# Performance work log

Hardware: AMD Instinct MI355X
Metric: run time of the kernel (lower is better)

Reference implementation:

```python
import jax, jax.numpy as jnp
import numpy as np

BN_EPS = 1e-3  # keras BatchNormalization default epsilon


def setup_inputs() -> dict:
    key = jax.random.key(0)
    ks = jax.random.split(key, 7)
    B, W, D, H, C = 2, 32, 32, 32, 256
    x = jax.random.normal(ks[0], (B, W, D, H, C), dtype=jnp.float32)
    # Stacked params for the 4 branches: [query, key, judge, value]
    conv_w = jax.random.normal(ks[1], (4, C, C), dtype=jnp.float32) / np.sqrt(C).astype(np.float32)
    conv_b = jax.random.normal(ks[2], (4, C), dtype=jnp.float32) * 0.01
    bn_scale = 1.0 + 0.1 * jax.random.normal(ks[3], (4, C), dtype=jnp.float32)
    bn_offset = 0.1 * jax.random.normal(ks[4], (4, C), dtype=jnp.float32)
    bn_mean = 0.1 * jax.random.normal(ks[5], (4, C), dtype=jnp.float32)
    bn_var = jax.random.uniform(ks[6], (4, C), dtype=jnp.float32, minval=0.5, maxval=1.5)
    gamma = jnp.asarray(1e-4, dtype=jnp.float32)  # scalar residual scale (init 0.0001 in source)
    return dict(x=x, conv_w=conv_w, conv_b=conv_b, bn_scale=bn_scale,
                bn_offset=bn_offset, bn_mean=bn_mean, bn_var=bn_var, gamma=gamma)


def _branch(x, w, b, s, o, m, v):
    # Conv3D 1x1x1 == per-voxel channel mixing, then inference-mode BN, then ReLU
    y = jnp.einsum('bwdhc,cf->bwdhf', x, w) + b
    y = s * (y - m) * jax.lax.rsqrt(v + BN_EPS) + o
    return jax.nn.relu(y)


def reference(x, conv_w, conv_b, bn_scale, bn_offset, bn_mean, bn_var, gamma):
    B, W, D, H, C = x.shape
    N = W * D * H
    # Raw reshape (B,W,D,H,C) -> (B,C,N), matching keras Reshape((C,-1)) on channels-last layout
    def br(i):
        return _branch(x, conv_w[i], conv_b[i], bn_scale[i], bn_offset[i],
                       bn_mean[i], bn_var[i]).reshape(B, C, N)
    Q, K, J, V = br(0), br(1), br(2), br(3)
    m1 = jnp.matmul(K, jnp.swapaxes(Q, 1, 2))   # (B, C, C)
    m2 = jnp.matmul(K, jnp.swapaxes(J, 1, 2))   # (B, C, C)
    affinity = jax.nn.sigmoid(jnp.matmul(m1, m2))  # (B, C, C), sigmoid not softmax
    weights = jnp.matmul(affinity, V)           # (B, C, N)
    weights = weights.reshape(B, W, D, H, C)    # raw reshape back, as in source
    return gamma * weights + x
```

## Files before the change

### kernel.cpp

```cpp
#include <hip/hip_runtime.h>
#include <math.h>

typedef __attribute__((ext_vector_type(4))) float  f32x4;
typedef __attribute__((ext_vector_type(8))) short  s16x8;
typedef __attribute__((ext_vector_type(4))) short  s16x4;

#define BN_EPS 1e-3f

static constexpr int    CC    = 256;
static constexpr int    NVOX  = 32768;
static constexpr int    BATCH = 2;
static constexpr int    MTOT  = BATCH * NVOX;
static constexpr size_t ELEM_BR = (size_t)MTOT * CC;
static constexpr size_t SZ_BR   = ELEM_BR * 2;
static constexpr size_t WS_Q   = 0;
static constexpr size_t WS_K   = WS_Q  + SZ_BR;
static constexpr size_t WS_J   = WS_K  + SZ_BR;
static constexpr size_t WS_V   = WS_J  + SZ_BR;
static constexpr size_t WS_M1  = WS_V  + SZ_BR;
static constexpr size_t WS_M2  = WS_M1 + (size_t)BATCH*CC*CC*4;
static constexpr size_t WS_AFF = WS_M2 + (size_t)BATCH*CC*CC*4;
static constexpr size_t WS_WT  = WS_AFF + (size_t)BATCH*CC*CC*2;
static constexpr size_t WS_AB  = WS_WT + (size_t)4*CC*CC*2;
static constexpr size_t WS_P   = WS_AB + 2048*4;
static constexpr size_t WS_NEED_PART = WS_P + (size_t)4*64*65536*2;

__device__ __forceinline__ short f2bf(float f) {
  union { float f; unsigned u; } v; v.f = f;
  unsigned u = v.u + 0x7FFFu + ((v.u >> 16) & 1u);
  return (short)(u >> 16);
}
__device__ __forceinline__ float bf2f(short s) {
  union { unsigned u; float f; } v; v.u = ((unsigned)(unsigned short)s) << 16;
  return v.f;
}

__global__ __launch_bounds__(256) void k0_prep(
    const float* __restrict__ conv_w, const float* __restrict__ conv_b,
    const float* __restrict__ bn_s, const float* __restrict__ bn_o,
    const float* __restrict__ bn_m, const float* __restrict__ bn_v,
    char* __restrict__ ws)
{
  int t = blockIdx.x * 256 + threadIdx.x;
  ((float*)(ws + WS_M1))[t] = 0.f;
  int f = t >> 16, rem = t & 65535;
  int cin = rem >> 8, cout = rem & 255;
  ((short*)(ws + WS_WT))[f*65536 + cout*256 + cin] = f2bf(conv_w[t]);
  if (t < 1024) {
    float alpha = bn_s[t] * rsqrtf(bn_v[t] + BN_EPS);
    float beta  = alpha * (conv_b[t] - bn_m[t]) + bn_o[t];
    float* ab = (float*)(ws + WS_AB);
    ab[t] = alpha; ab[1024 + t] = beta;
  }
}

__global__ __launch_bounds__(256, 2) void k1_branches(
    const float* __restrict__ x, char* __restrict__ ws)
{
  __shared__ short As[64 * 256];
  __shared__ short Bs[64 * 256];
  __shared__ short Rs[64][72];

  const int tid = threadIdx.x;
  const int m0  = blockIdx.x * 64;
  const int lane = tid & 63, wid = tid >> 6;
  const int wm = wid >> 1, wn = wid & 1;
  const int lr = lane & 15, lg = lane >> 4;

  const short* Wt = (const short*)(ws + WS_WT);
  const float* ab = (const float*)(ws + WS_AB);

  #pragma unroll
  for (int it = 0; it < 16; ++it) {
    int idx = tid + 256 * it;
    int r = idx >> 6, c4 = (idx & 63) << 2;
    const float4 v = *(const float4*)(x + (size_t)(m0 + r) * 256 + c4);
    s16x4 s; s[0]=f2bf(v.x); s[1]=f2bf(v.y); s[2]=f2bf(v.z); s[3]=f2bf(v.w);
    int u = c4 >> 3;
    int swz = ((u ^ ((r & 7) << 2)) << 3) | (c4 & 7);
    *(s16x4*)&As[r * 256 + swz] = s;
  }

  {
    const short* Wf = Wt;
    #pragma unroll
    for (int i = 0; i < 8; ++i) {
      int slot = i * 256 + tid;
      int cout = slot >> 5, u = slot & 31;
      int usrc = u ^ ((cout & 7) << 2);
      const short* src = Wf + cout * 256 + usrc * 8;
      short* dst = Bs + (size_t)(i * 256 + wid * 64) * 8;
      __builtin_amdgcn_global_load_lds(
          (const __attribute__((address_space(1))) void*)src,
          (__attribute__((address_space(3))) void*)dst, 16, 0, 0);
    }
  }

  __syncthreads();

  for (int nt = 0; nt < 16; ++nt) {
    const int f  = nt >> 2;
    const int c0 = (nt & 3) * 64;

    f32x4 acc[2][2];
    #pragma unroll
    for (int a = 0; a < 2; ++a)
      #pragma unroll
      for (int b = 0; b < 2; ++b) { f32x4 z = {0.f,0.f,0.f,0.f}; acc[a][b] = z; }

    #pragma unroll
    for (int k0 = 0; k0 < 8; ++k0) {
      const int ua = k0 * 4 + lg;
      s16x8 af[2], bf[2];
      #pragma unroll
      for (int mi = 0; mi < 2; ++mi) {
        int r = wm*32 + mi*16 + lr;
        int uu = ua ^ ((r & 7) << 2);
        af[mi] = *(const s16x8*)&As[r * 256 + uu * 8];
      }
      #pragma unroll
      for (int nj = 0; nj < 2; ++nj) {
        int c = wn*32 + nj*16 + lr;
        int uu = ua ^ ((c & 7) << 2);
        bf[nj] = *(const s16x8*)&Bs[c * 256 + uu * 8];
      }
      #pragma unroll
      for (int mi = 0; mi < 2; ++mi)
        #pragma unroll
        for (int nj = 0; nj < 2; ++nj)
          acc[mi][nj] = __builtin_amdgcn_mfma_f32_16x16x32_bf16(
              bf[nj], af[mi], acc[mi][nj], 0, 0, 0);
    }

    __syncthreads();

    if (nt < 15) {
      const int fn  = (nt + 1) >> 2;
      const int c0n = ((nt + 1) & 3) * 64;
      const short* Wf = Wt + fn * 65536 + c0n * 256;
      #pragma unroll
      for (int i = 0; i < 8; ++i) {
        int slot = i * 256 + tid;
        int cout = slot >> 5, u = slot & 31;
        int usrc = u ^ ((cout & 7) << 2);
        const short* src = Wf + cout * 256 + usrc * 8;
        short* dst = Bs + (size_t)(i * 256 + wid * 64) * 8;
        __builtin_amdgcn_global_load_lds(
            (const __attribute__((address_space(1))) void*)src,
            (__attribute__((address_space(3))) void*)dst, 16, 0, 0);
      }
    }

    #pragma unroll
    for (int nj = 0; nj < 2; ++nj) {
      int c4b = c0 + wn*32 + nj*16 + lg*4;
      const f32x4 al = *(const f32x4*)&ab[f*256 + c4b];
      const f32x4 be = *(const f32x4*)&ab[1024 + f*256 + c4b];
      #pragma unroll
      for (int mi = 0; mi < 2; ++mi) {
        s16x4 s;
        #pragma unroll
        for (int ii = 0; ii < 4; ++ii) {
          float yv = al[ii] * acc[mi][nj][ii] + be[ii];
          yv = yv > 0.f ? yv : 0.f;
          s[ii] = f2bf(yv);
        }
        *(s16x4*)&Rs[wm*32 + mi*16 + lr][wn*32 + nj*16 + lg*4] = s;
      }
    }

    __syncthreads();

    short* Yf = (short*)(ws + (size_t)f * SZ_BR);
    #pragma unroll
    for (int it = 0; it < 2; ++it) {
      int idx = tid + 256 * it;
      int r = idx >> 3, c8 = (idx & 7) << 3;
      *(s16x8*)&Yf[(size_t)(m0 + r) * 256 + c0 + c8] = *(const s16x8*)&Rs[r][c8];
    }
  }
}

template<int PART>
__global__ __launch_bounds__(512, 2) void k2_m1m2(char* __restrict__ ws)
{
  __shared__ short Ks[2][16384];
  __shared__ short Xs[2][16384];

  const int tid = threadIdx.x;
  const int chunk = blockIdx.x;
  const int mat = blockIdx.y;
  const int b   = blockIdx.z;
  const size_t boff = (size_t)b * NVOX * CC;
  const short* Km = (const short*)(ws + WS_K) + boff;
  const short* Xm = (const short*)(ws + (mat ? WS_J : WS_Q)) + boff;

  const int lane = tid & 63, wid = tid >> 6;
  const int wm = wid >> 1, wn = wid & 1;
  const int lr = lane & 15, lg = lane >> 4;

  f32x4 acc[4][8];
  #pragma unroll
  for (int a = 0; a < 4; ++a)
    #pragma unroll
    for (int c = 0; c < 8; ++c) { f32x4 z = {0.f,0.f,0.f,0.f}; acc[a][c] = z; }

  {
    const int n0 = chunk * 512;
    #pragma unroll
    for (int i = 0; i < 4; ++i) {
      int slot = i * 512 + tid;
      int r = slot >> 3, u = slot & 7;
      int usrc = u ^ (r & 7);
      const size_t so = (size_t)r * NVOX + n0 + usrc * 8;
      short* dK = Ks[0] + (size_t)(i * 512 + wid * 64) * 8;
      short* dX = Xs[0] + (size_t)(i * 512 + wid * 64) * 8;
      __builtin_amdgcn_global_load_lds(
          (const __attribute__((address_space(1))) void*)(Km + so),
          (__attribute__((address_space(3))) void*)dK, 16, 0, 0);
      __builtin_amdgcn_global_load_lds(
          (const __attribute__((address_space(1))) void*)(Xm + so),
          (__attribute__((address_space(3))) void*)dX, 16, 0, 0);
    }
  }
  __syncthreads();

  for (int t = 0; t < 8; ++t) {
    const int cur = t & 1;
    if (t < 7) {
      const int n0n = chunk * 512 + (t + 1) * 64;
      const int nxt = cur ^ 1;
      #pragma unroll
      for (int i = 0; i < 4; ++i) {
        int slot = i * 512 + tid;
        int r = slot >> 3, u = slot & 7;
        int usrc = u ^ (r & 7);
        const size_t so = (size_t)r * NVOX + n0n + usrc * 8;
        short* dK = Ks[nxt] + (size_t)(i * 512 + wid * 64) * 8;
        short* dX = Xs[nxt] + (size_t)(i * 512 + wid * 64) * 8;
        __builtin_amdgcn_global_load_lds(
            (const __attribute__((address_space(1))) void*)(Km + so),
            (__attribute__((address_space(3))) void*)dK, 16, 0, 0);
        __builtin_amdgcn_global_load_lds(
            (const __attribute__((address_space(1))) void*)(Xm + so),
            (__attribute__((address_space(3))) void*)dX, 16, 0, 0);
      }
    }
    #pragma unroll
    for (int ks = 0; ks < 2; ++ks) {
      const int ua = ks * 4 + lg;
      s16x8 a[4], xf[8];
      #pragma unroll
      for (int mi = 0; mi < 4; ++mi) {
        int r = wm*64 + mi*16 + lr;
        a[mi] = *(const s16x8*)&Ks[cur][r * 64 + (ua ^ (r & 7)) * 8];
      }
      #pragma unroll
      for (int nj = 0; nj < 8; ++nj) {
        int r = wn*128 + nj*16 + lr;
        xf[nj] = *(const s16x8*)&Xs[cur][r * 64 + (ua ^ (r & 7)) * 8];
      }
      #pragma unroll
      for (int mi = 0; mi < 4; ++mi)
        #pragma unroll
        for (int nj = 0; nj < 8; ++nj)
          acc[mi][nj] = __builtin_amdgcn_mfma_f32_16x16x32_bf16(
              a[mi], xf[nj], acc[mi][nj], 0, 0, 0);
    }
    __syncthreads();
  }

  if (PART) {
    short* P = (short*)(ws + WS_P) + ((size_t)((mat*2 + b)*64 + chunk)) * 65536;
    #pragma unroll
    for (int mi = 0; mi < 4; ++mi)
      #pragma unroll
      for (int nj = 0; nj < 8; ++nj) {
        int i = wm*64 + mi*16 + lg*4;
        int j = wn*128 + nj*16 + lr;
        #pragma unroll
        for (int ii = 0; ii < 4; ++ii)
          P[(size_t)(i + ii) * 256 + j] = f2bf(acc[mi][nj][ii]);
      }
  } else {
    float* M = (float*)(ws + (mat ? WS_M2 : WS_M1)) + (size_t)b * CC * CC;
    #pragma unroll
    for (int mi = 0; mi < 4; ++mi)
      #pragma unroll
      for (int nj = 0; nj < 8; ++nj) {
        int i = wm*64 + mi*16 + lg*4;
        int j = wn*128 + nj*16 + lr;
        #pragma unroll
        for (int ii = 0; ii < 4; ++ii)
          atomicAdd(&M[(size_t)(i + ii) * 256 + j], acc[mi][nj][ii]);
      }
  }
}

__global__ __launch_bounds__(256) void k25_reduce(char* __restrict__ ws)
{
  int idx = blockIdx.x * 256 + threadIdx.x;
  int mb = idx >> 16;
  int ij = idx & 65535;
  const short* P = (const short*)(ws + WS_P) + ((size_t)mb * 64) * 65536 + ij;
  float s = 0.f;
  #pragma unroll 8
  for (int c = 0; c < 64; ++c)
    s += bf2f(P[(size_t)c * 65536]);
  float* dst = (float*)(ws + ((mb >> 1) ? WS_M2 : WS_M1)) + (size_t)(mb & 1) * 65536 + ij;
  *dst = s;
}

__global__ __launch_bounds__(256) void k3_aff(char* __restrict__ ws)
{
  const int j = threadIdx.x;
  const int i = blockIdx.x & 255;
  const int b = blockIdx.x >> 8;
  const float* m1 = (const float*)(ws + WS_M1) + (size_t)b * CC * CC;
  const float* m2 = (const float*)(ws + WS_M2) + (size_t)b * CC * CC;
  float z = 0.f;
  #pragma unroll 8
  for (int k = 0; k < 256; ++k)
    z = fmaf(m1[i*256 + k], m2[k*256 + j], z);
  float a = 1.f / (1.f + expf(-z));
  ((short*)(ws + WS_AFF))[(size_t)b*CC*CC + i*256 + j] = f2bf(a);
}

__global__ __launch_bounds__(512, 4) void k4_out(
    const float* __restrict__ x, const float* __restrict__ gamma_p,
    char* __restrict__ ws, float* __restrict__ out)
{
  __shared__ short affS[256][72];
  __shared__ short Vs[128][72];

  const int tid = threadIdx.x;
  const int n0 = blockIdx.x * 128;
  const int b  = blockIdx.y;
  const float gamma = gamma_p[0];
  const short* aff = (const short*)(ws + WS_AFF) + (size_t)b * CC * CC;
  const short* Vm  = (const short*)(ws + WS_V) + (size_t)b * NVOX * CC;

  const int lane = tid & 63, wid = tid >> 6;
  const int wi = wid >> 1, wn = wid & 1;
  const int lr = lane & 15, lg = lane >> 4;

  f32x4 acc[4][4];
  #pragma unroll
  for (int a = 0; a < 4; ++a)
    #pragma unroll
    for (int c = 0; c < 4; ++c) { f32x4 z = {0.f,0.f,0.f,0.f}; acc[a][c] = z; }

  for (int c0 = 0; c0 < 256; c0 += 64) {
    __syncthreads();
    #pragma unroll
    for (int it = 0; it < 4; ++it) {
      int idx = tid + 512 * it;
      int r = idx >> 3, c8 = (idx & 7) << 3;
      *(s16x8*)&affS[r][c8] = *(const s16x8*)&aff[(size_t)r * 256 + c0 + c8];
    }
    #pragma unroll
    for (int it = 0; it < 2; ++it) {
      int idx = tid + 512 * it;
      int t15 = idx & 15;
      int cc = idx >> 4, n8 = t15 << 3;
      s16x8 v = *(const s16x8*)&Vm[(size_t)(c0 + cc) * NVOX + n0 + n8];
      #pragma unroll
      for (int uu = 0; uu < 8; ++uu) {
        int u = (uu + t15) & 7;
        Vs[n8 + u][cc] = v[u];
      }
    }
    __syncthreads();
    #pragma unroll
    for (int ks = 0; ks < 2; ++ks) {
      s16x8 af[4], bv[4];
      #pragma unroll
      for (int mi = 0; mi < 4; ++mi)
        af[mi] = *(const s16x8*)&affS[wi*64 + mi*16 + lr][ks*32 + lg*8];
      #pragma unroll
      for (int nj = 0; nj < 4; ++nj)
        bv[nj] = *(const s16x8*)&Vs[wn*64 + nj*16 + lr][ks*32 + lg*8];
      #pragma unroll
      for (int mi = 0; mi < 4; ++mi)
        #pragma unroll
        for (int nj = 0; nj < 4; ++nj)
          acc[mi][nj] = __builtin_amdgcn_mfma_f32_16x16x32_bf16(
              bv[nj], af[mi], acc[mi][nj], 0, 0, 0);
    }
  }
  #pragma unroll
  for (int mi = 0; mi < 4; ++mi)
    #pragma unroll
    for (int nj = 0; nj < 4; ++nj) {
      int i = wi*64 + mi*16 + lr;
      int n = n0 + wn*64 + nj*16 + lg*4;
      size_t flat = (size_t)b * NVOX * CC + (size_t)i * NVOX + n;
      const float4 xv = *(const float4*)(x + flat);
      float4 o;
      o.x = gamma * acc[mi][nj][0] + xv.x;
      o.y = gamma * acc[mi][nj][1] + xv.y;
      o.z = gamma * acc[mi][nj][2] + xv.z;
      o.w = gamma * acc[mi][nj][3] + xv.w;
      *(float4*)(out + flat) = o;
    }
}

extern "C" void kernel_launch(void* const* d_in, const int* in_sizes, int n_in,
                              void* d_out, int out_size, void* d_ws, size_t ws_size,
                              hipStream_t stream)
{
  const float* x      = (const float*)d_in[0];
  const float* conv_w = (const float*)d_in[1];
  const float* conv_b = (const float*)d_in[2];
  const float* bn_s   = (const float*)d_in[3];
  const float* bn_o   = (const float*)d_in[4];
  const float* bn_m   = (const float*)d_in[5];
  const float* bn_v   = (const float*)d_in[6];
  const float* gamma  = (const float*)d_in[7];
  char*  ws  = (char*)d_ws;
  float* out = (float*)d_out;

  const bool part = ws_size >= WS_NEED_PART;

  k0_prep    <<<1024, 256, 0, stream>>>(conv_w, conv_b, bn_s, bn_o, bn_m, bn_v, ws);
  k1_branches<<<1024, 256, 0, stream>>>(x, ws);
  if (part) {
    k2_m1m2<1><<<dim3(64, 2, 2), 512, 0, stream>>>(ws);
    k25_reduce<<<1024, 256, 0, stream>>>(ws);
  } else {
    k2_m1m2<0><<<dim3(64, 2, 2), 512, 0, stream>>>(ws);
  }
  k3_aff     <<<512, 256, 0, stream>>>(ws);
  k4_out     <<<dim3(256, 2), 512, 0, stream>>>(x, gamma, ws, out);
}
```

Baseline: 166.6 us.

## Restructure branch GEMM with double-buffered weights, register-resident A, shuffle-based stores

```diff
diff --git a/kernel.cpp b/kernel.cpp
--- a/kernel.cpp
+++ b/kernel.cpp
@@ -34,6 +34,15 @@
   union { unsigned u; float f; } v; v.u = ((unsigned)(unsigned short)s) << 16;
   return v.f;
 }
+__device__ __forceinline__ unsigned long long packBN(f32x4 a, f32x4 al, f32x4 be) {
+  union { s16x4 v; unsigned long long u; } c;
+  #pragma unroll
+  for (int ii = 0; ii < 4; ++ii) {
+    float yv = al[ii] * a[ii] + be[ii];
+    c.v[ii] = f2bf(yv > 0.f ? yv : 0.f);
+  }
+  return c.u;
+}
 
 __global__ __launch_bounds__(256) void k0_prep(
     const float* __restrict__ conv_w, const float* __restrict__ conv_b,
@@ -54,130 +63,123 @@
   }
 }
 
-__global__ __launch_bounds__(256, 2) void k1_branches(
+__global__ __launch_bounds__(512, 1) void k1_branches(
     const float* __restrict__ x, char* __restrict__ ws)
 {
-  __shared__ short As[64 * 256];
-  __shared__ short Bs[64 * 256];
-  __shared__ short Rs[64][72];
+  __shared__ short As[128 * 256];
+  __shared__ short Bs[2][64 * 256];
 
   const int tid = threadIdx.x;
-  const int m0  = blockIdx.x * 64;
+  const int m0  = blockIdx.x * 128;
   const int lane = tid & 63, wid = tid >> 6;
-  const int wm = wid >> 1, wn = wid & 1;
+  const int rowg = wid >> 1, coutg = wid & 1;
   const int lr = lane & 15, lg = lane >> 4;
 
   const short* Wt = (const short*)(ws + WS_WT);
   const float* ab = (const float*)(ws + WS_AB);
 
   #pragma unroll
+  for (int i = 0; i < 4; ++i) {
+    int slot = i * 512 + tid;
+    int cout = slot >> 5, u = slot & 31;
+    int usrc = u ^ (cout & 7);
+    __builtin_amdgcn_global_load_lds(
+        (const __attribute__((address_space(1))) void*)(Wt + cout * 256 + usrc * 8),
+        (__attribute__((address_space(3))) void*)(&Bs[0][(i * 512 + wid * 64) * 8]),
+        16, 0, 0);
+  }
+
+  #pragma unroll
   for (int it = 0; it < 16; ++it) {
-    int idx = tid + 256 * it;
+    int idx = tid + 512 * it;
     int r = idx >> 6, c4 = (idx & 63) << 2;
     const float4 v = *(const float4*)(x + (size_t)(m0 + r) * 256 + c4);
     s16x4 s; s[0]=f2bf(v.x); s[1]=f2bf(v.y); s[2]=f2bf(v.z); s[3]=f2bf(v.w);
     int u = c4 >> 3;
-    int swz = ((u ^ ((r & 7) << 2)) << 3) | (c4 & 7);
+    int swz = ((u ^ (r & 7)) << 3) | (c4 & 7);
     *(s16x4*)&As[r * 256 + swz] = s;
   }
 
-  {
-    const short* Wf = Wt;
-    #pragma unroll
-    for (int i = 0; i < 8; ++i) {
-      int slot = i * 256 + tid;
-      int cout = slot >> 5, u = slot & 31;
-      int usrc = u ^ ((cout & 7) << 2);
-      const short* src = Wf + cout * 256 + usrc * 8;
-      short* dst = Bs + (size_t)(i * 256 + wid * 64) * 8;
-      __builtin_amdgcn_global_load_lds(
-          (const __attribute__((address_space(1))) void*)src,
-          (__attribute__((address_space(3))) void*)dst, 16, 0, 0);
-    }
-  }
-
   __syncthreads();
+
+  const int rA0 = rowg * 32 + lr, rA1 = rA0 + 16;
+#define LDA(R, K) (*(const s16x8*)&As[(R) * 256 + ((((K)*4 + lg) ^ ((R) & 7)) * 8)])
+  const s16x8 fa00 = LDA(rA0,0), fa01 = LDA(rA0,1), fa02 = LDA(rA0,2), fa03 = LDA(rA0,3);
+  const s16x8 fa04 = LDA(rA0,4), fa05 = LDA(rA0,5), fa06 = LDA(rA0,6), fa07 = LDA(rA0,7);
+  const s16x8 fa10 = LDA(rA1,0), fa11 = LDA(rA1,1), fa12 = LDA(rA1,2), fa13 = LDA(rA1,3);
+  const s16x8 fa14 = LDA(rA1,4), fa15 = LDA(rA1,5), fa16 = LDA(rA1,6), fa17 = LDA(rA1,7);
+#undef LDA
+
+  const int cB0 = coutg * 32 + lr, cB1 = cB0 + 16;
 
   for (int nt = 0; nt < 16; ++nt) {
     const int f  = nt >> 2;
     const int c0 = (nt & 3) * 64;
 
-    f32x4 acc[2][2];
-    #pragma unroll
-    for (int a = 0; a < 2; ++a)
-      #pragma unroll
-      for (int b = 0; b < 2; ++b) { f32x4 z = {0.f,0.f,0.f,0.f}; acc[a][b] = z; }
-
-    #pragma unroll
-    for (int k0 = 0; k0 < 8; ++k0) {
-      const int ua = k0 * 4 + lg;
-      s16x8 af[2], bf[2];
-      #pragma unroll
-      for (int mi = 0; mi < 2; ++mi) {
-        int r = wm*32 + mi*16 + lr;
-        int uu = ua ^ ((r & 7) << 2);
-        af[mi] = *(const s16x8*)&As[r * 256 + uu * 8];
-      }
-      #pragma unroll
-      for (int nj = 0; nj < 2; ++nj) {
-        int c = wn*32 + nj*16 + lr;
-        int uu = ua ^ ((c & 7) << 2);
-        bf[nj] = *(const s16x8*)&Bs[c * 256 + uu * 8];
-      }
-      #pragma unroll
-      for (int mi = 0; mi < 2; ++mi)
-        #pragma unroll
-        for (int nj = 0; nj < 2; ++nj)
-          acc[mi][nj] = __builtin_amdgcn_mfma_f32_16x16x32_bf16(
-              bf[nj], af[mi], acc[mi][nj], 0, 0, 0);
+    if (nt < 15) {
+      const int ntn = nt + 1;
+      const short* Wf = Wt + (ntn >> 2) * 65536 + ((ntn & 3) * 64) * 256;
+      short* Bn = Bs[ntn & 1];
+      #pragma unroll
+      for (int i = 0; i < 4; ++i) {
+        int slot = i * 512 + tid;
+        int cout = slot >> 5, u = slot & 31;
+        int usrc = u ^ (cout & 7);
+        __builtin_amdgcn_global_load_lds(
+            (const __attribute__((address_space(1))) void*)(Wf + cout * 256 + usrc * 8),
+            (__attribute__((address_space(3))) void*)(&Bn[(i * 512 + wid * 64) * 8]),
+            16, 0, 0);
+      }
+    }
+
+    const short* Bc = Bs[nt & 1];
+    f32x4 acc00 = {0.f,0.f,0.f,0.f}, acc01 = {0.f,0.f,0.f,0.f};
+    f32x4 acc10 = {0.f,0.f,0.f,0.f}, acc11 = {0.f,0.f,0.f,0.f};
+#define KST(K, A0, A1) { \
+    const int ua_ = (K) * 4 + lg; \
+    const s16x8 b0_ = *(const s16x8*)&Bc[cB0 * 256 + ((ua_ ^ (cB0 & 7)) * 8)]; \
+    const s16x8 b1_ = *(const s16x8*)&Bc[cB1 * 256 + ((ua_ ^ (cB1 & 7)) * 8)]; \
+    acc00 = __builtin_amdgcn_mfma_f32_16x16x32_bf16(b0_, (A0), acc00, 0,0,0); \
+    acc01 = __builtin_amdgcn_mfma_f32_16x16x32_bf16(b1_, (A0), acc01, 0,0,0); \
+    acc10 = __builtin_amdgcn_mfma_f32_16x16x32_bf16(b0_, (A1), acc10, 0,0,0); \
+    acc11 = __builtin_amdgcn_mfma_f32_16x16x32_bf16(b1_, (A1), acc11, 0,0,0); }
+    KST(0, fa00, fa10) KST(1, fa01, fa11) KST(2, fa02, fa12) KST(3, fa03, fa13)
+    KST(4, fa04, fa14) KST(5, fa05, fa15) KST(6, fa06, fa16) KST(7, fa07, fa17)
+#undef KST
+
+    short* Yf = (short*)(ws + (size_t)f * SZ_BR);
+    {
+      const int cbase = c0 + coutg * 32;
+      const f32x4 al0 = *(const f32x4*)&ab[f*256 + cbase + lg*4];
+      const f32x4 be0 = *(const f32x4*)&ab[1024 + f*256 + cbase + lg*4];
+      const f32x4 al1 = *(const f32x4*)&ab[f*256 + cbase + 16 + lg*4];
+      const f32x4 be1 = *(const f32x4*)&ab[1024 + f*256 + cbase + 16 + lg*4];
+      const int cout_s = cbase + (lg & 1) * 16 + (lg >> 1) * 8;
+      {
+        unsigned long long p0 = packBN(acc00, al0, be0);
+        unsigned long long p1 = packBN(acc01, al1, be1);
+        unsigned long long q0 = __shfl_xor(p0, 16, 64);
+        unsigned long long q1 = __shfl_xor(p1, 16, 64);
+        ulonglong2 ch0, ch1;
+        if (lg & 1) { ch0.x = q0; ch0.y = p0; ch1.x = q1; ch1.y = p1; }
+        else        { ch0.x = p0; ch0.y = q0; ch1.x = p1; ch1.y = q1; }
+        ulonglong2 sel = (lg & 1) ? ch1 : ch0;
+        *(ulonglong2*)&Yf[(size_t)(m0 + rowg*32 + lr) * 256 + cout_s] = sel;
+      }
+      {
+        unsigned long long p0 = packBN(acc10, al0, be0);
+        unsigned long long p1 = packBN(acc11, al1, be1);
+        unsigned long long q0 = __shfl_xor(p0, 16, 64);
+        unsigned long long q1 = __shfl_xor(p1, 16, 64);
+        ulonglong2 ch0, ch1;
+        if (lg & 1) { ch0.x = q0; ch0.y = p0; ch1.x = q1; ch1.y = p1; }
+        else        { ch0.x = p0; ch0.y = q0; ch1.x = p1; ch1.y = q1; }
+        ulonglong2 sel = (lg & 1) ? ch1 : ch0;
+        *(ulonglong2*)&Yf[(size_t)(m0 + rowg*32 + 16 + lr) * 256 + cout_s] = sel;
+      }
     }
 
     __syncthreads();
-
-    if (nt < 15) {
-      const int fn  = (nt + 1) >> 2;
-      const int c0n = ((nt + 1) & 3) * 64;
-      const short* Wf = Wt + fn * 65536 + c0n * 256;
-      #pragma unroll
-      for (int i = 0; i < 8; ++i) {
-        int slot = i * 256 + tid;
-        int cout = slot >> 5, u = slot & 31;
-        int usrc = u ^ ((cout & 7) << 2);
-        const short* src = Wf + cout * 256 + usrc * 8;
-        short* dst = Bs + (size_t)(i * 256 + wid * 64) * 8;
-        __builtin_amdgcn_global_load_lds(
-            (const __attribute__((address_space(1))) void*)src,
-            (__attribute__((address_space(3))) void*)dst, 16, 0, 0);
-      }
-    }
-
-    #pragma unroll
-    for (int nj = 0; nj < 2; ++nj) {
-      int c4b = c0 + wn*32 + nj*16 + lg*4;
-      const f32x4 al = *(const f32x4*)&ab[f*256 + c4b];
-      const f32x4 be = *(const f32x4*)&ab[1024 + f*256 + c4b];
-      #pragma unroll
-      for (int mi = 0; mi < 2; ++mi) {
-        s16x4 s;
-        #pragma unroll
-        for (int ii = 0; ii < 4; ++ii) {
-          float yv = al[ii] * acc[mi][nj][ii] + be[ii];
-          yv = yv > 0.f ? yv : 0.f;
-          s[ii] = f2bf(yv);
-        }
-        *(s16x4*)&Rs[wm*32 + mi*16 + lr][wn*32 + nj*16 + lg*4] = s;
-      }
-    }
-
-    __syncthreads();
-
-    short* Yf = (short*)(ws + (size_t)f * SZ_BR);
-    #pragma unroll
-    for (int it = 0; it < 2; ++it) {
-      int idx = tid + 256 * it;
-      int r = idx >> 3, c8 = (idx & 7) << 3;
-      *(s16x8*)&Yf[(size_t)(m0 + r) * 256 + c0 + c8] = *(const s16x8*)&Rs[r][c8];
-    }
   }
 }
 
@@ -423,7 +425,7 @@
   const bool part = ws_size >= WS_NEED_PART;
 
   k0_prep    <<<1024, 256, 0, stream>>>(conv_w, conv_b, bn_s, bn_o, bn_m, bn_v, ws);
-  k1_branches<<<1024, 256, 0, stream>>>(x, ws);
+  k1_branches<<<512, 512, 0, stream>>>(x, ws);
   if (part) {
     k2_m1m2<1><<<dim3(64, 2, 2), 512, 0, stream>>>(ws);
     k25_reduce<<<1024, 256, 0, stream>>>(ws);
```

New measurement: 208.5 us. +25.2%, slower.

## Split branch projection into bf16 convert pass plus 128x128-tiled pipelined GEMM

Applied to the files above, without the earlier changes.

```diff
diff --git a/kernel.cpp b/kernel.cpp
--- a/kernel.cpp
+++ b/kernel.cpp
@@ -6,6 +6,8 @@
 typedef __attribute__((ext_vector_type(4))) short  s16x4;
 
 #define BN_EPS 1e-3f
+#define AS1 const __attribute__((address_space(1))) void*
+#define AS3 __attribute__((address_space(3))) void*
 
 static constexpr int    CC    = 256;
 static constexpr int    NVOX  = 32768;
@@ -34,6 +36,15 @@
   union { unsigned u; float f; } v; v.u = ((unsigned)(unsigned short)s) << 16;
   return v.f;
 }
+__device__ __forceinline__ unsigned long long packBN(f32x4 a, f32x4 al, f32x4 be) {
+  union { s16x4 v; unsigned long long u; } c;
+  #pragma unroll
+  for (int ii = 0; ii < 4; ++ii) {
+    float yv = al[ii] * a[ii] + be[ii];
+    c.v[ii] = f2bf(yv > 0.f ? yv : 0.f);
+  }
+  return c.u;
+}
 
 __global__ __launch_bounds__(256) void k0_prep(
     const float* __restrict__ conv_w, const float* __restrict__ conv_b,
@@ -54,6 +65,125 @@
   }
 }
 
+__global__ __launch_bounds__(256) void k0b_convert(
+    const float* __restrict__ x, char* __restrict__ ws)
+{
+  int t = blockIdx.x * 256 + threadIdx.x;
+  short* Xbf = (short*)(ws + WS_P);
+  #pragma unroll
+  for (int it = 0; it < 16; ++it) {
+    int f4 = t + 262144 * it;
+    const float4 v = *(const float4*)(x + (size_t)f4 * 4);
+    s16x4 s; s[0]=f2bf(v.x); s[1]=f2bf(v.y); s[2]=f2bf(v.z); s[3]=f2bf(v.w);
+    *(s16x4*)&Xbf[(size_t)f4 * 4] = s;
+  }
+}
+
+__global__ __launch_bounds__(256, 2) void k1b_gemm(char* __restrict__ ws)
+{
+  __shared__ short Aa[2][128 * 64];
+  __shared__ short Wl[2][128 * 64];
+
+  const int tid = threadIdx.x;
+  const int bid = blockIdx.x;
+  const int r8 = bid & 7, q = bid >> 3;
+  const int cg = q & 7, rt = (q >> 3) * 8 + r8;
+  const int f  = cg >> 1, c0 = (cg & 1) * 128;
+
+  const short* Xbf = (const short*)(ws + WS_P);
+  const short* Wf  = (const short*)(ws + WS_WT) + f * 65536;
+  const float* ab  = (const float*)(ws + WS_AB);
+
+  const int lane = tid & 63, wid = tid >> 6;
+  const int wm = wid >> 1, wn = wid & 1;
+  const int lr = lane & 15, lg = lane >> 4;
+
+  #pragma unroll
+  for (int i = 0; i < 4; ++i) {
+    int slot = i * 256 + tid;
+    int r = slot >> 3, u = slot & 7, us = u ^ (r & 7);
+    __builtin_amdgcn_global_load_lds(
+        (AS1)(Xbf + (size_t)(rt*128 + r) * 256 + us * 8),
+        (AS3)(&Aa[0][(i * 256 + wid * 64) * 8]), 16, 0, 0);
+    __builtin_amdgcn_global_load_lds(
+        (AS1)(Wf + (c0 + r) * 256 + us * 8),
+        (AS3)(&Wl[0][(i * 256 + wid * 64) * 8]), 16, 0, 0);
+  }
+  __syncthreads();
+
+  f32x4 acc[4][4];
+  #pragma unroll
+  for (int a = 0; a < 4; ++a)
+    #pragma unroll
+    for (int c = 0; c < 4; ++c) { f32x4 z = {0.f,0.f,0.f,0.f}; acc[a][c] = z; }
+
+  for (int kt = 0; kt < 4; ++kt) {
+    const int cur = kt & 1;
+    if (kt < 3) {
+      const int ko = (kt + 1) * 64;
+      const int nxt = cur ^ 1;
+      #pragma unroll
+      for (int i = 0; i < 4; ++i) {
+        int slot = i * 256 + tid;
+        int r = slot >> 3, u = slot & 7, us = u ^ (r & 7);
+        __builtin_amdgcn_global_load_lds(
+            (AS1)(Xbf + (size_t)(rt*128 + r) * 256 + ko + us * 8),
+            (AS3)(&Aa[nxt][(i * 256 + wid * 64) * 8]), 16, 0, 0);
+        __builtin_amdgcn_global_load_lds(
+            (AS1)(Wf + (c0 + r) * 256 + ko + us * 8),
+            (AS3)(&Wl[nxt][(i * 256 + wid * 64) * 8]), 16, 0, 0);
+      }
+    }
+    #pragma unroll
+    for (int ks = 0; ks < 2; ++ks) {
+      const int ua = ks * 4 + lg;
+      s16x8 af[4], wf[4];
+      #pragma unroll
+      for (int mi = 0; mi < 4; ++mi) {
+        int r = wm*64 + mi*16 + lr;
+        af[mi] = *(const s16x8*)&Aa[cur][r * 64 + (ua ^ (r & 7)) * 8];
+      }
+      #pragma unroll
+      for (int nj = 0; nj < 4; ++nj) {
+        int c = wn*64 + nj*16 + lr;
+        wf[nj] = *(const s16x8*)&Wl[cur][c * 64 + (ua ^ (c & 7)) * 8];
+      }
+      #pragma unroll
+      for (int mi = 0; mi < 4; ++mi)
+        #pragma unroll
+        for (int nj = 0; nj < 4; ++nj)
+          acc[mi][nj] = __builtin_amdgcn_mfma_f32_16x16x32_bf16(
+              wf[nj], af[mi], acc[mi][nj], 0, 0, 0);
+    }
+    __syncthreads();
+  }
+
+  short* Yf = (short*)(ws + (size_t)f * SZ_BR);
+  const int cwb = c0 + wn * 64;
+  #pragma unroll
+  for (int mi = 0; mi < 4; ++mi) {
+    const size_t row = (size_t)(rt*128 + wm*64 + mi*16 + lr);
+    #pragma unroll
+    for (int njp = 0; njp < 4; njp += 2) {
+      const int ca = cwb + njp*16 + lg*4;
+      const f32x4 al0 = *(const f32x4*)&ab[f*256 + ca];
+      const f32x4 be0 = *(const f32x4*)&ab[1024 + f*256 + ca];
+      const f32x4 al1 = *(const f32x4*)&ab[f*256 + ca + 16];
+      const f32x4 be1 = *(const f32x4*)&ab[1024 + f*256 + ca + 16];
+      unsigned long long p0 = packBN(acc[mi][njp],     al0, be0);
+      unsigned long long p1 = packBN(acc[mi][njp + 1], al1, be1);
+      unsigned long long q0 = __shfl_xor(p0, 16, 64);
+      unsigned long long q1 = __shfl_xor(p1, 16, 64);
+      ulonglong2 ch0, ch1;
+      if (lg & 1) { ch0.x = q0; ch0.y = p0; ch1.x = q1; ch1.y = p1; }
+      else        { ch0.x = p0; ch0.y = q0; ch1.x = p1; ch1.y = q1; }
+      ulonglong2 sel = (lg & 1) ? ch1 : ch0;
+      const int cout_s = cwb + njp*16 + (lg & 1) * 16 + (lg >> 1) * 8;
+      *(ulonglong2*)&Yf[row * 256 + cout_s] = sel;
+    }
+  }
+}
+
 __global__ __launch_bounds__(256, 2) void k1_branches(
     const float* __restrict__ x, char* __restrict__ ws)
 {
@@ -80,34 +210,27 @@
     int swz = ((u ^ ((r & 7) << 2)) << 3) | (c4 & 7);
     *(s16x4*)&As[r * 256 + swz] = s;
   }
-
   {
-    const short* Wf = Wt;
     #pragma unroll
     for (int i = 0; i < 8; ++i) {
       int slot = i * 256 + tid;
       int cout = slot >> 5, u = slot & 31;
       int usrc = u ^ ((cout & 7) << 2);
-      const short* src = Wf + cout * 256 + usrc * 8;
-      short* dst = Bs + (size_t)(i * 256 + wid * 64) * 8;
       __builtin_amdgcn_global_load_lds(
-          (const __attribute__((address_space(1))) void*)src,
-          (__attribute__((address_space(3))) void*)dst, 16, 0, 0);
-    }
-  }
-
+          (AS1)(Wt + cout * 256 + usrc * 8),
+          (AS3)(Bs + (size_t)(i * 256 + wid * 64) * 8), 16, 0, 0);
+    }
+  }
   __syncthreads();
 
   for (int nt = 0; nt < 16; ++nt) {
     const int f  = nt >> 2;
     const int c0 = (nt & 3) * 64;
-
     f32x4 acc[2][2];
     #pragma unroll
     for (int a = 0; a < 2; ++a)
       #pragma unroll
       for (int b = 0; b < 2; ++b) { f32x4 z = {0.f,0.f,0.f,0.f}; acc[a][b] = z; }
-
     #pragma unroll
     for (int k0 = 0; k0 < 8; ++k0) {
       const int ua = k0 * 4 + lg;
@@ -115,14 +238,12 @@
       #pragma unroll
       for (int mi = 0; mi < 2; ++mi) {
         int r = wm*32 + mi*16 + lr;
-        int uu = ua ^ ((r & 7) << 2);
-        af[mi] = *(const s16x8*)&As[r * 256 + uu * 8];
+        af[mi] = *(const s16x8*)&As[r * 256 + (ua ^ ((r & 7) << 2)) * 8];
       }
       #pragma unroll
       for (int nj = 0; nj < 2; ++nj) {
         int c = wn*32 + nj*16 + lr;
-        int uu = ua ^ ((c & 7) << 2);
-        bf[nj] = *(const s16x8*)&Bs[c * 256 + uu * 8];
+        bf[nj] = *(const s16x8*)&Bs[c * 256 + (ua ^ ((c & 7) << 2)) * 8];
       }
       #pragma unroll
       for (int mi = 0; mi < 2; ++mi)
@@ -131,26 +252,21 @@
           acc[mi][nj] = __builtin_amdgcn_mfma_f32_16x16x32_bf16(
               bf[nj], af[mi], acc[mi][nj], 0, 0, 0);
     }
-
     __syncthreads();
-
     if (nt < 15) {
       const int fn  = (nt + 1) >> 2;
       const int c0n = ((nt + 1) & 3) * 64;
-      const short* Wf = Wt + fn * 65536 + c0n * 256;
+      const short* Wfp = Wt + fn * 65536 + c0n * 256;
       #pragma unroll
       for (int i = 0; i < 8; ++i) {
         int slot = i * 256 + tid;
         int cout = slot >> 5, u = slot & 31;
         int usrc = u ^ ((cout & 7) << 2);
-        const short* src = Wf + cout * 256 + usrc * 8;
-        short* dst = Bs + (size_t)(i * 256 + wid * 64) * 8;
         __builtin_amdgcn_global_load_lds(
-            (const __attribute__((address_space(1))) void*)src,
-            (__attribute__((address_space(3))) void*)dst, 16, 0, 0);
-      }
-    }
-
+            (AS1)(Wfp + cout * 256 + usrc * 8),
+            (AS3)(Bs + (size_t)(i * 256 + wid * 64) * 8), 16, 0, 0);
+      }
+    }
     #pragma unroll
     for (int nj = 0; nj < 2; ++nj) {
       int c4b = c0 + wn*32 + nj*16 + lg*4;
@@ -168,9 +284,7 @@
         *(s16x4*)&Rs[wm*32 + mi*16 + lr][wn*32 + nj*16 + lg*4] = s;
       }
     }
-
     __syncthreads();
-
     short* Yf = (short*)(ws + (size_t)f * SZ_BR);
     #pragma unroll
     for (int it = 0; it < 2; ++it) {
@@ -213,14 +327,10 @@
       int r = slot >> 3, u = slot & 7;
       int usrc = u ^ (r & 7);
       const size_t so = (size_t)r * NVOX + n0 + usrc * 8;
-      short* dK = Ks[0] + (size_t)(i * 512 + wid * 64) * 8;
-      short* dX = Xs[0] + (size_t)(i * 512 + wid * 64) * 8;
-      __builtin_amdgcn_global_load_lds(
-          (const __attribute__((address_space(1))) void*)(Km + so),
-          (__attribute__((address_space(3))) void*)dK, 16, 0, 0);
-      __builtin_amdgcn_global_load_lds(
-          (const __attribute__((address_space(1))) void*)(Xm + so),
-          (__attribute__((address_space(3))) void*)dX, 16, 0, 0);
+      __builtin_amdgcn_global_load_lds((AS1)(Km + so),
+          (AS3)(Ks[0] + (size_t)(i * 512 + wid * 64) * 8), 16, 0, 0);
+      __builtin_amdgcn_global_load_lds((AS1)(Xm + so),
+          (AS3)(Xs[0] + (size_t)(i * 512 + wid * 64) * 8), 16, 0, 0);
     }
   }
   __syncthreads();
@@ -236,14 +346,10 @@
         int r = slot >> 3, u = slot & 7;
         int usrc = u ^ (r & 7);
         const size_t so = (size_t)r * NVOX + n0n + usrc * 8;
-        short* dK = Ks[nxt] + (size_t)(i * 512 + wid * 64) * 8;
-        short* dX = Xs[nxt] + (size_t)(i * 512 + wid * 64) * 8;
-        __builtin_amdgcn_global_load_lds(
-            (const __attribute__((address_space(1))) void*)(Km + so),
-            (__attribute__((address_space(3))) void*)dK, 16, 0, 0);
-        __builtin_amdgcn_global_load_lds(
-            (const __attribute__((address_space(1))) void*)(Xm + so),
-            (__attribute__((address_space(3))) void*)dX, 16, 0, 0);
+        __builtin_amdgcn_global_load_lds((AS1)(Km + so),
+            (AS3)(Ks[nxt] + (size_t)(i * 512 + wid * 64) * 8), 16, 0, 0);
+        __builtin_amdgcn_global_load_lds((AS1)(Xm + so),
+            (AS3)(Xs[nxt] + (size_t)(i * 512 + wid * 64) * 8), 16, 0, 0);
       }
     }
     #pragma unroll
@@ -423,12 +529,14 @@
   const bool part = ws_size >= WS_NEED_PART;
 
   k0_prep    <<<1024, 256, 0, stream>>>(conv_w, conv_b, bn_s, bn_o, bn_m, bn_v, ws);
-  k1_branches<<<1024, 256, 0, stream>>>(x, ws);
   if (part) {
-    k2_m1m2<1><<<dim3(64, 2, 2), 512, 0, stream>>>(ws);
-    k25_reduce<<<1024, 256, 0, stream>>>(ws);
+    k0b_convert<<<1024, 256, 0, stream>>>(x, ws);
+    k1b_gemm   <<<4096, 256, 0, stream>>>(ws);
+    k2_m1m2<1> <<<dim3(64, 2, 2), 512, 0, stream>>>(ws);
+    k25_reduce <<<1024, 256, 0, stream>>>(ws);
   } else {
-    k2_m1m2<0><<<dim3(64, 2, 2), 512, 0, stream>>>(ws);
+    k1_branches<<<1024, 256, 0, stream>>>(x, ws);
+    k2_m1m2<0> <<<dim3(64, 2, 2), 512, 0, stream>>>(ws);
   }
   k3_aff     <<<512, 256, 0, stream>>>(ws);
   k4_out     <<<dim3(256, 2), 512, 0, stream>>>(x, gamma, ws, out);
```

After: 223.1 us. 1.34x slower.
